# Optimization experiments

Hardware: AMD Instinct MI355X
Metric: run time of the kernel (lower is better)

## Reference

```python
import jax, jax.numpy as jnp
import numpy as np

FC = 2048      # fc_feat_size
VEMB = 512     # video_embedding_size
WEMB = 512     # word_embedding_size
H = 512        # lstm_hidden_size
A = 256        # att_hidden_size
TV = 32        # video_time_step
TC = 20        # caption_time_step
BC = 16        # batch_size_caption
RP = 32        # rp_num (proposals per caption)
B = BC * RP    # batch_size
GLOVE = 300


def setup_inputs() -> dict:
    key = jax.random.key(0)
    ks = jax.random.split(key, 12)
    def u(k, shape):
        return jax.random.uniform(k, shape, jnp.float32, -0.1, 0.1)
    def n(k, shape, s=0.05):
        return jax.random.normal(k, shape, jnp.float32) * s
    return {
        "video_fc_feat": jax.random.normal(ks[0], (B, TV, FC), jnp.float32),
        "video_caption": jax.random.normal(ks[1], (BC, TC, GLOVE), jnp.float32),
        "cap_length_list": jax.random.randint(ks[2], (BC,), 0, TC),
        # video_embedding / word_embedding (Linear layers)
        "W_vemb": u(ks[3], (VEMB, FC)), "b_vemb": jnp.zeros((VEMB,), jnp.float32),
        "W_wemb": u(ks[4], (WEMB, GLOVE)), "b_wemb": jnp.zeros((WEMB,), jnp.float32),
        # LSTMCell for video (gate order i,f,g,o as in torch)
        "Wih_v": n(ks[5], (4 * H, VEMB)), "Whh_v": n(ks[6], (4 * H, H)),
        "bih_v": jnp.zeros((4 * H,), jnp.float32), "bhh_v": jnp.zeros((4 * H,), jnp.float32),
        # LSTMCell for caption
        "Wih_c": n(ks[7], (4 * H, WEMB)), "Whh_c": n(ks[8], (4 * H, H)),
        "bih_c": jnp.zeros((4 * H,), jnp.float32), "bhh_c": jnp.zeros((4 * H,), jnp.float32),
        # attention linears
        "W_vid": u(ks[9], (A, H)), "b_vid": jnp.zeros((A,), jnp.float32),
        "W_sen": u(ks[10], (A, H)), "b_sen": jnp.zeros((A,), jnp.float32),
        "W_att": u(ks[11], (1, A)), "b_att": jnp.zeros((1,), jnp.float32),
    }


def _lstm(x_seq, Wih, Whh, bih, bhh):
    # x_seq: [B, T, D] -> hidden states [B, T, H]; torch LSTMCell gate order i,f,g,o
    Bb = x_seq.shape[0]
    Hh = Whh.shape[1]
    def step(carry, x):
        h, c = carry
        g = x @ Wih.T + bih + h @ Whh.T + bhh
        i, f, gg, o = jnp.split(g, 4, axis=-1)
        c = jax.nn.sigmoid(f) * c + jax.nn.sigmoid(i) * jnp.tanh(gg)
        h = jax.nn.sigmoid(o) * jnp.tanh(c)
        return (h, c), h
    init = (jnp.zeros((Bb, Hh), x_seq.dtype), jnp.zeros((Bb, Hh), x_seq.dtype))
    _, hs = jax.lax.scan(step, init, jnp.swapaxes(x_seq, 0, 1))
    return jnp.swapaxes(hs, 0, 1)


def reference(video_fc_feat, video_caption, cap_length_list,
              W_vemb, b_vemb, W_wemb, b_wemb,
              Wih_v, Whh_v, bih_v, bhh_v,
              Wih_c, Whh_c, bih_c, bhh_c,
              W_vid, b_vid, W_sen, b_sen, W_att, b_att):
    Bb, TVv, _ = video_fc_feat.shape
    BCc, TCc, _ = video_caption.shape
    rp = Bb // BCc
    Hh = Whh_v.shape[1]

    # caption LSTM over embedded GloVe words
    cap_x = video_caption @ W_wemb.T + b_wemb                 # [BC, TC, WEMB]
    cap_h = _lstm(cap_x, Wih_c, Whh_c, bih_c, bhh_c)          # [BC, TC, H]
    # video LSTM over embedded fc features
    vid_x = video_fc_feat @ W_vemb.T + b_vemb                 # [B, TV, VEMB]
    vid_h = _lstm(vid_x, Wih_v, Whh_v, bih_v, bhh_v)          # [B, TV, H]

    # additive attention: tanh(vid_linear(h_v) + sen_linear(h_c)) -> att_linear
    c_lin = cap_h @ W_sen.T + b_sen                           # [BC, TC, A]
    v_lin = (vid_h @ W_vid.T + b_vid).reshape(BCc, rp, TVv, -1)  # [BC, RP, TV, A]
    scores = (jnp.tanh(v_lin[:, :, :, None, :] + c_lin[:, None, None, :, :])
              @ W_att.T + b_att)[..., 0]                      # [BC, RP, TV, TC]

    # ragged masked softmax over caption length (max(len, 1) as in original)
    cap_len = jnp.maximum(cap_length_list, 1)
    mask = jnp.arange(TCc)[None, :] < cap_len[:, None]        # [BC, TC]
    m = mask[:, None, None, :]
    w = jax.nn.softmax(jnp.where(m, scores, -1e9), axis=-1)
    w = jnp.where(m, w, 0.0)                                  # [BC, RP, TV, TC]

    att_cap = jnp.einsum('brvt,bth->brvh', w, cap_h)          # [BC, RP, TV, H]
    cap_ftr_mean = att_cap.mean(axis=2)                       # mean over video steps
    vid_mean = vid_h.mean(axis=1).reshape(BCc, rp, Hh)
    return (vid_mean, cap_ftr_mean)
```

## Files before the change

### kernel.cpp

```cpp
#include <hip/hip_runtime.h>
#include <hip/hip_bf16.h>

#define FCD 2048
#define VEMBD 512
#define WEMBD 512
#define HD 512
#define AD 256
#define TVD 32
#define TCD 20
#define BCD 16
#define RPD 32
#define BD 512
#define GLOVED 300

typedef __attribute__((ext_vector_type(8))) short short8v;
typedef __attribute__((ext_vector_type(4))) float f32x4;

__device__ __forceinline__ float sigf(float x) { return 1.0f / (1.0f + __expf(-x)); }
__device__ __forceinline__ float tanhfast(float x) {
    float e = __expf(2.0f * x);
    return 1.0f - 2.0f / (e + 1.0f);
}
__device__ __forceinline__ unsigned short f2bf(float x) {
    union { __hip_bfloat16 h; unsigned short u; } v;
    v.h = __float2bfloat16(x);
    return v.u;
}
__device__ __forceinline__ float b2f(unsigned short u) {
    union { unsigned int i; float f; } v;
    v.i = ((unsigned int)u) << 16;
    return v.f;
}

__launch_bounds__(256)
__global__ void conv_f2b_kernel(const float* __restrict__ src,
                                unsigned short* __restrict__ dst, int n4) {
    for (int i = blockIdx.x * 256 + threadIdx.x; i < n4; i += gridDim.x * 256) {
        const float4 v = ((const float4*)src)[i];
        ushort4 o;
        o.x = f2bf(v.x); o.y = f2bf(v.y); o.z = f2bf(v.z); o.w = f2bf(v.w);
        ((ushort4*)dst)[i] = o;
    }
}

__launch_bounds__(256)
__global__ void conv_wcat_perm_kernel(const float* __restrict__ Wih,
                                      const float* __restrict__ Whh,
                                      unsigned short* __restrict__ Wcat) {
    const int gp = blockIdx.x;
    const int q = (gp >> 4) & 3;
    const int hc = (gp >> 6) * 16 + (gp & 15);
    const long g = (long)(q * 512 + hc);
    for (int k = threadIdx.x; k < 512; k += 256) {
        Wcat[(long)gp * 1024 + k]       = f2bf(Wih[g * 512 + k]);
        Wcat[(long)gp * 1024 + 512 + k] = f2bf(Whh[g * 512 + k]);
    }
}

__launch_bounds__(256)
__global__ void conv_bsum_kernel(const float* __restrict__ bih,
                                 const float* __restrict__ bhh,
                                 float* __restrict__ bsum) {
    const int gp = blockIdx.x * 256 + threadIdx.x;
    if (gp < 2048) {
        const int q = (gp >> 4) & 3;
        const int hc = (gp >> 6) * 16 + (gp & 15);
        const int g = q * 512 + hc;
        bsum[gp] = bih[g] + bhh[g];
    }
}

template<int AF32, int OBF>
__launch_bounds__(256)
__global__ void mfma_gemm128(const void* __restrict__ A,
                             const unsigned short* __restrict__ Bw,
                             const float* __restrict__ bias,
                             void* __restrict__ Cout,
                             int M, int N, int K)
{
    __shared__ unsigned short As[128][72];
    __shared__ unsigned short Bs[128][72];
    const int m0 = blockIdx.x * 128;
    const int n0 = blockIdx.y * 128;
    const int tid = threadIdx.x;
    const int lane = tid & 63;
    const int wid = tid >> 6;
    const int wm = (wid >> 1) * 64;
    const int wn = (wid & 1) * 64;
    const int lrow = lane & 15;
    const int lko = (lane >> 4) * 8;
    const int sr = tid >> 1;
    const int sc = (tid & 1) * 32;

    f32x4 acc[4][4] = {};

    const float* Arow_f = (const float*)A + (long)(m0 + sr) * K;
    const unsigned short* Arow_b = (const unsigned short*)A + (long)(m0 + sr) * K;
    const unsigned short* Brow = Bw + (long)(n0 + sr) * K;

    if (AF32) {
#pragma unroll
        for (int i = 0; i < 8; i++) {
            const float4 v = *(const float4*)(Arow_f + sc + i * 4);
            unsigned short* d = &As[sr][sc + i * 4];
            d[0] = f2bf(v.x); d[1] = f2bf(v.y); d[2] = f2bf(v.z); d[3] = f2bf(v.w);
        }
    } else {
#pragma unroll
        for (int i = 0; i < 4; i++)
            *(short8v*)&As[sr][sc + i * 8] = *(const short8v*)(Arow_b + sc + i * 8);
    }
#pragma unroll
    for (int i = 0; i < 4; i++)
        *(short8v*)&Bs[sr][sc + i * 8] = *(const short8v*)(Brow + sc + i * 8);
    __syncthreads();

    const int nc = K >> 6;
    float4 paf[8];
    short8v pab[4], pb[4];
    for (int c = 0; c < nc; c++) {
        if (c < nc - 1) {
            const int k0 = (c + 1) * 64;
            if (AF32) {
#pragma unroll
                for (int i = 0; i < 8; i++)
                    paf[i] = *(const float4*)(Arow_f + k0 + sc + i * 4);
            } else {
#pragma unroll
                for (int i = 0; i < 4; i++)
                    pab[i] = *(const short8v*)(Arow_b + k0 + sc + i * 8);
            }
#pragma unroll
            for (int i = 0; i < 4; i++)
                pb[i] = *(const short8v*)(Brow + k0 + sc + i * 8);
        }
#pragma unroll
        for (int kk = 0; kk < 2; kk++) {
            short8v a[4], b[4];
#pragma unroll
            for (int mi = 0; mi < 4; mi++)
                a[mi] = *(const short8v*)&As[wm + mi * 16 + lrow][kk * 32 + lko];
#pragma unroll
            for (int ni = 0; ni < 4; ni++)
                b[ni] = *(const short8v*)&Bs[wn + ni * 16 + lrow][kk * 32 + lko];
#pragma unroll
            for (int mi = 0; mi < 4; mi++)
#pragma unroll
                for (int ni = 0; ni < 4; ni++)
                    acc[mi][ni] = __builtin_amdgcn_mfma_f32_16x16x32_bf16(
                        a[mi], b[ni], acc[mi][ni], 0, 0, 0);
        }
        __syncthreads();
        if (c < nc - 1) {
            if (AF32) {
#pragma unroll
                for (int i = 0; i < 8; i++) {
                    unsigned short* d = &As[sr][sc + i * 4];
                    d[0] = f2bf(paf[i].x); d[1] = f2bf(paf[i].y);
                    d[2] = f2bf(paf[i].z); d[3] = f2bf(paf[i].w);
                }
            } else {
#pragma unroll
                for (int i = 0; i < 4; i++)
                    *(short8v*)&As[sr][sc + i * 8] = pab[i];
            }
#pragma unroll
            for (int i = 0; i < 4; i++)
                *(short8v*)&Bs[sr][sc + i * 8] = pb[i];
            __syncthreads();
        }
    }

    const int rbase = (lane >> 4) * 4;
#pragma unroll
    for (int ni = 0; ni < 4; ni++) {
        const int col = n0 + wn + ni * 16 + lrow;
        const float bv = bias[col];
#pragma unroll
        for (int mi = 0; mi < 4; mi++) {
#pragma unroll
            for (int j = 0; j < 4; j++) {
                const long row = m0 + wm + mi * 16 + rbase + j;
                const float val = acc[mi][ni][j] + bv;
                if (OBF) ((unsigned short*)Cout)[row * N + col] = f2bf(val);
                else     ((float*)Cout)[row * N + col] = val;
            }
        }
    }
}

__launch_bounds__(256, 2)
__global__ void step_fused(const unsigned short* __restrict__ vx,
                           const unsigned short* __restrict__ h_in,
                           unsigned short* __restrict__ h_out,
                           const unsigned short* __restrict__ Wcat,
                           const float* __restrict__ bsum,
                           float* __restrict__ c_state,
                           unsigned short* __restrict__ vid_h,
                           int t,
                           const float* __restrict__ xg,
                           const float* __restrict__ Whh_c,
                           const float* __restrict__ bhh_c,
                           const float* __restrict__ hc_in,
                           float* __restrict__ hc_out,
                           float* __restrict__ cap_cst,
                           float* __restrict__ cap_h)
{
    __shared__ __align__(16) unsigned char smem[26112];
    const int bx = blockIdx.x;
    const int tid = threadIdx.x;

    if (bx >= 512) {
        const int h0 = (bx - 512) * 16;
        float* Wsc = (float*)smem;
        float* Hshc = (float*)(smem + 17408);
        const int tx = tid & 15;
        const int ty = tid >> 4;
        const int lrow2 = tid >> 2;
        const int lq = tid & 3;
        float acc4[4] = {};

        for (int k0 = 0; k0 < 512; k0 += 64) {
            {
                const int q = lrow2 >> 4;
                const int hcc = lrow2 & 15;
                const float* src = Whh_c + (long)(q * 512 + h0 + hcc) * 512 + k0 + lq * 16;
                const int col = hcc * 4 + q;
#pragma unroll
                for (int j = 0; j < 4; j++) {
                    const float4 v = *(const float4*)(src + j * 4);
                    Wsc[(lq * 16 + j * 4 + 0) * 68 + col] = v.x;
                    Wsc[(lq * 16 + j * 4 + 1) * 68 + col] = v.y;
                    Wsc[(lq * 16 + j * 4 + 2) * 68 + col] = v.z;
                    Wsc[(lq * 16 + j * 4 + 3) * 68 + col] = v.w;
                }
            }
            {
                const int lb = tid >> 4;
                const int lk4 = (tid & 15) * 4;
                *(float4*)&Hshc[lb * 68 + lk4] = *(const float4*)(hc_in + (long)lb * 512 + k0 + lk4);
            }
            __syncthreads();
#pragma unroll
            for (int kq = 0; kq < 16; kq++) {
                const float4 h4 = *(const float4*)&Hshc[ty * 68 + kq * 4];
                const float4 w0 = *(const float4*)&Wsc[(kq * 4 + 0) * 68 + tx * 4];
                const float4 w1 = *(const float4*)&Wsc[(kq * 4 + 1) * 68 + tx * 4];
                const float4 w2 = *(const float4*)&Wsc[(kq * 4 + 2) * 68 + tx * 4];
                const float4 w3 = *(const float4*)&Wsc[(kq * 4 + 3) * 68 + tx * 4];
                acc4[0] += h4.x * w0.x + h4.y * w1.x + h4.z * w2.x + h4.w * w3.x;
                acc4[1] += h4.x * w0.y + h4.y * w1.y + h4.z * w2.y + h4.w * w3.y;
                acc4[2] += h4.x * w0.z + h4.y * w1.z + h4.z * w2.z + h4.w * w3.z;
                acc4[3] += h4.x * w0.w + h4.y * w1.w + h4.z * w2.w + h4.w * w3.w;
            }
            __syncthreads();
        }
        const int hc = h0 + tx;
        const long xrow = (long)(ty * TCD + t) * 2048;
        const float gi = acc4[0] + xg[xrow + hc]        + bhh_c[hc];
        const float gf = acc4[1] + xg[xrow + 512 + hc]  + bhh_c[512 + hc];
        const float gg = acc4[2] + xg[xrow + 1024 + hc] + bhh_c[1024 + hc];
        const float go = acc4[3] + xg[xrow + 1536 + hc] + bhh_c[1536 + hc];
        const float c_old = cap_cst[(long)ty * 512 + hc];
        const float ii = sigf(gi), ff = sigf(gf), g2 = tanhfast(gg), oo = sigf(go);
        const float c = ff * c_old + ii * g2;
        const float h = oo * tanhfast(c);
        cap_cst[(long)ty * 512 + hc] = c;
        hc_out[(long)ty * 512 + hc] = h;
        cap_h[(long)(ty * TCD + t) * 512 + hc] = h;
        return;
    }

    const int n0 = (bx & 31) * 64;
    const int b0 = (bx >> 5) * 32;
    const int lane = tid & 63;
    const int w = tid >> 6;
    const int bi = w & 1;
    const int nq = w >> 1;
    const int lrow = lane & 15;
    const int lko = (lane >> 4) * 8;
    const int sra = tid >> 3;
    const int sca = (tid & 7) * 16;

    unsigned short* As = (unsigned short*)smem;
    unsigned short* Ws = (unsigned short*)(smem + 8704);

    const unsigned short* arow_vx = vx + ((long)(b0 + sra) * TVD + t) * 512;
    const unsigned short* arow_h  = h_in + (long)(b0 + sra) * 512;
    const unsigned short* wrow0   = Wcat + (long)(n0 + sra) * 1024;
    const unsigned short* wrow1   = Wcat + (long)(n0 + sra + 32) * 1024;

    f32x4 acc[2] = {};

    *(short8v*)&As[sra * 136 + sca]     = *(const short8v*)(arow_vx + sca);
    *(short8v*)&As[sra * 136 + sca + 8] = *(const short8v*)(arow_vx + sca + 8);
    *(short8v*)&Ws[sra * 136 + sca]            = *(const short8v*)(wrow0 + sca);
    *(short8v*)&Ws[sra * 136 + sca + 8]        = *(const short8v*)(wrow0 + sca + 8);
    *(short8v*)&Ws[(sra + 32) * 136 + sca]     = *(const short8v*)(wrow1 + sca);
    *(short8v*)&Ws[(sra + 32) * 136 + sca + 8] = *(const short8v*)(wrow1 + sca + 8);
    __syncthreads();

    short8v pa0, pa1, pw0, pw1, pw2, pw3;
    for (int c = 0; c < 8; c++) {
        if (c < 7) {
            const int k0 = (c + 1) * 128;
            const unsigned short* ap = (k0 < 512) ? (arow_vx + k0) : (arow_h + (k0 - 512));
            pa0 = *(const short8v*)(ap + sca);
            pa1 = *(const short8v*)(ap + sca + 8);
            pw0 = *(const short8v*)(wrow0 + k0 + sca);
            pw1 = *(const short8v*)(wrow0 + k0 + sca + 8);
            pw2 = *(const short8v*)(wrow1 + k0 + sca);
            pw3 = *(const short8v*)(wrow1 + k0 + sca + 8);
        }
#pragma unroll
        for (int kk = 0; kk < 4; kk++) {
            const short8v a = *(const short8v*)&As[(bi * 16 + lrow) * 136 + kk * 32 + lko];
#pragma unroll
            for (int nl = 0; nl < 2; nl++) {
                const short8v b = *(const short8v*)&Ws[((nq * 2 + nl) * 16 + lrow) * 136 + kk * 32 + lko];
                acc[nl] = __builtin_amdgcn_mfma_f32_16x16x32_bf16(a, b, acc[nl], 0, 0, 0);
            }
        }
        __syncthreads();
        if (c < 7) {
            *(short8v*)&As[sra * 136 + sca]            = pa0;
            *(short8v*)&As[sra * 136 + sca + 8]        = pa1;
            *(short8v*)&Ws[sra * 136 + sca]            = pw0;
            *(short8v*)&Ws[sra * 136 + sca + 8]        = pw1;
            *(short8v*)&Ws[(sra + 32) * 136 + sca]     = pw2;
            *(short8v*)&Ws[(sra + 32) * 136 + sca + 8] = pw3;
            __syncthreads();
        }
    }

    float* red = (float*)smem;
    const int rbase = (lane >> 4) * 4;
    if (w >= 2) {
#pragma unroll
        for (int nl = 0; nl < 2; nl++)
#pragma unroll
            for (int j = 0; j < 4; j++)
                red[nl * 512 + (bi * 16 + rbase + j) * 16 + lrow] = acc[nl][j];
    }
    __syncthreads();
    if (w < 2) {
        const int hc = (n0 >> 2) + lrow;
        const float bs0 = bsum[n0 + lrow];
        const float bs1 = bsum[n0 + 16 + lrow];
        const float bs2 = bsum[n0 + 32 + lrow];
        const float bs3 = bsum[n0 + 48 + lrow];
#pragma unroll
        for (int j = 0; j < 4; j++) {
            const int blocal = bi * 16 + rbase + j;
            const long b = b0 + blocal;
            const float gi = acc[0][j] + bs0;
            const float gf = acc[1][j] + bs1;
            const float gg = red[blocal * 16 + lrow] + bs2;
            const float go = red[512 + blocal * 16 + lrow] + bs3;
            const float c_old = c_state[b * 512 + hc];
            const float ii = sigf(gi), ff = sigf(gf), g2 = tanhfast(gg), oo = sigf(go);
            const float cn = ff * c_old + ii * g2;
            const float h = oo * tanhfast(cn);
            c_state[b * 512 + hc] = cn;
            h_out[b * 512 + hc] = f2bf(h);
            vid_h[(b * TVD + t) * 512 + hc] = f2bf(h);
        }
    }
}

__launch_bounds__(256)
__global__ void gemm_bias_kernel(const float* __restrict__ A,
                                 const float* __restrict__ Bw,
                                 const float* __restrict__ bias,
                                 float* __restrict__ C,
                                 int M, int N, int K) {
    __shared__ float As[16][68];
    __shared__ float Bs[16][68];
    const int n0 = blockIdx.x * 64;
    const int m0 = blockIdx.y * 64;
    const int tid = threadIdx.x;
    const int tx = tid & 15;
    const int ty = tid >> 4;
    const int lrow = tid >> 2;
    const int lk4 = (tid & 3) * 4;

    float acc[4][4] = {};

    for (int k0 = 0; k0 < K; k0 += 16) {
        {
            const float* src = A + (long)(m0 + lrow) * K + k0 + lk4;
            float4 v;
            if (k0 + 16 <= K) v = *(const float4*)src;
            else {
                v.x = (k0 + lk4 + 0 < K) ? src[0] : 0.f;
                v.y = (k0 + lk4 + 1 < K) ? src[1] : 0.f;
                v.z = (k0 + lk4 + 2 < K) ? src[2] : 0.f;
                v.w = (k0 + lk4 + 3 < K) ? src[3] : 0.f;
            }
            As[lk4 + 0][lrow] = v.x; As[lk4 + 1][lrow] = v.y;
            As[lk4 + 2][lrow] = v.z; As[lk4 + 3][lrow] = v.w;
        }
        {
            const float* src = Bw + (long)(n0 + lrow) * K + k0 + lk4;
            float4 v;
            if (k0 + 16 <= K) v = *(const float4*)src;
            else {
                v.x = (k0 + lk4 + 0 < K) ? src[0] : 0.f;
                v.y = (k0 + lk4 + 1 < K) ? src[1] : 0.f;
                v.z = (k0 + lk4 + 2 < K) ? src[2] : 0.f;
                v.w = (k0 + lk4 + 3 < K) ? src[3] : 0.f;
            }
            Bs[lk4 + 0][lrow] = v.x; Bs[lk4 + 1][lrow] = v.y;
            Bs[lk4 + 2][lrow] = v.z; Bs[lk4 + 3][lrow] = v.w;
        }
        __syncthreads();
#pragma unroll
        for (int kk = 0; kk < 16; kk++) {
            const float4 av = *(const float4*)&As[kk][ty * 4];
            const float4 bv = *(const float4*)&Bs[kk][tx * 4];
            acc[0][0] += av.x * bv.x; acc[0][1] += av.x * bv.y; acc[0][2] += av.x * bv.z; acc[0][3] += av.x * bv.w;
            acc[1][0] += av.y * bv.x; acc[1][1] += av.y * bv.y; acc[1][2] += av.y * bv.z; acc[1][3] += av.y * bv.w;
            acc[2][0] += av.z * bv.x; acc[2][1] += av.z * bv.y; acc[2][2] += av.z * bv.z; acc[2][3] += av.z * bv.w;
            acc[3][0] += av.w * bv.x; acc[3][1] += av.w * bv.y; acc[3][2] += av.w * bv.z; acc[3][3] += av.w * bv.w;
        }
        __syncthreads();
    }

    const float b0v = bias[n0 + tx * 4 + 0];
    const float b1v = bias[n0 + tx * 4 + 1];
    const float b2v = bias[n0 + tx * 4 + 2];
    const float b3v = bias[n0 + tx * 4 + 3];
#pragma unroll
    for (int i = 0; i < 4; i++) {
        float* dst = C + (long)(m0 + ty * 4 + i) * N + n0 + tx * 4;
        dst[0] = acc[i][0] + b0v;
        dst[1] = acc[i][1] + b1v;
        dst[2] = acc[i][2] + b2v;
        dst[3] = acc[i][3] + b3v;
    }
}

#define PFL 258
__launch_bounds__(256, 2)
__global__ void attn_kernel(const float* __restrict__ v_lin,
                            const float* __restrict__ c_lin,
                            const float* __restrict__ W_att,
                            const float* __restrict__ b_att,
                            const int* __restrict__ cap_len,
                            const float* __restrict__ cap_h,
                            float* __restrict__ out2)
{
    const int br = blockIdx.x;
    const int bc = br >> 5;
    const int tid = threadIdx.x;
    __shared__ float cl[TCD][PFL];
    __shared__ float vl[TVD][PFL];
    __shared__ float wa[AD];
    __shared__ float sl[TVD][TCD];
    __shared__ float wsum[TCD];

    {
        const float* csrc = c_lin + (long)bc * TCD * AD;
        for (int idx = tid; idx < TCD * 128; idx += 256) {
            const int row = idx >> 7, c2 = (idx & 127) * 2;
            *(float2*)&cl[row][c2] = *(const float2*)(csrc + row * AD + c2);
        }
        const float* vsrc = v_lin + (long)br * TVD * AD;
        for (int idx = tid; idx < TVD * 128; idx += 256) {
            const int row = idx >> 7, c2 = (idx & 127) * 2;
            *(float2*)&vl[row][c2] = *(const float2*)(vsrc + row * AD + c2);
        }
        wa[tid] = W_att[tid];
    }
    const float batt = b_att[0];
    __syncthreads();

    {
        const int v = tid & 31;
        const int tg = tid >> 5;
        const int t0 = tg, t1 = tg + 8, t2 = tg + 16;
        const bool ok2 = (t2 < TCD);
        const int t2c = ok2 ? t2 : 0;
        float s0 = 0.f, s1 = 0.f, s2 = 0.f;
#pragma unroll 4
        for (int i = 0; i < 128; i++) {
            const float2 w2 = *(const float2*)&wa[2 * i];
            const float2 vv = *(const float2*)&vl[v][2 * i];
            const float2 c0 = *(const float2*)&cl[t0][2 * i];
            const float2 c1 = *(const float2*)&cl[t1][2 * i];
            const float2 c2 = *(const float2*)&cl[t2c][2 * i];
            s0 += tanhfast(vv.x + c0.x) * w2.x + tanhfast(vv.y + c0.y) * w2.y;
            s1 += tanhfast(vv.x + c1.x) * w2.x + tanhfast(vv.y + c1.y) * w2.y;
            s2 += tanhfast(vv.x + c2.x) * w2.x + tanhfast(vv.y + c2.y) * w2.y;
        }
        sl[v][t0] = s0 + batt;
        sl[v][t1] = s1 + batt;
        if (ok2) sl[v][t2] = s2 + batt;
    }
    __syncthreads();

    int L = cap_len[bc];
    if (L < 1) L = 1;
    if (tid < TVD) {
        const int v = tid;
        float m = -1e30f;
        for (int t = 0; t < TCD; t++)
            if (t < L) m = fmaxf(m, sl[v][t]);
        float sum = 0.f;
        for (int t = 0; t < TCD; t++)
            if (t < L) sum += __expf(sl[v][t] - m);
        const float inv = 1.f / sum;
        for (int t = 0; t < TCD; t++)
            sl[v][t] = (t < L) ? __expf(sl[v][t] - m) * inv : 0.f;
    }
    __syncthreads();
    if (tid < TCD) {
        float s = 0.f;
        for (int v = 0; v < TVD; v++) s += sl[v][tid];
        wsum[tid] = s * (1.0f / TVD);
    }
    __syncthreads();

    const float* chb = cap_h + (long)bc * TCD * HD;
#pragma unroll
    for (int r = 0; r < 2; r++) {
        const int h = r * 256 + tid;
        float s = 0.f;
#pragma unroll
        for (int t = 0; t < TCD; t++)
            s += wsum[t] * chb[t * HD + h];
        out2[(long)br * HD + h] = s;
    }
}

__launch_bounds__(256)
__global__ void vidmean_bf_kernel(const unsigned short* __restrict__ vid_h,
                                  float* __restrict__ out1)
{
    const int idx = blockIdx.x * 256 + threadIdx.x;
    const int b = idx >> 6;
    const int h8 = (idx & 63) * 8;
    float s[8] = {};
    for (int t = 0; t < TVD; t++) {
        const short8v v = *(const short8v*)(vid_h + ((long)b * TVD + t) * 512 + h8);
#pragma unroll
        for (int j = 0; j < 8; j++) s[j] += b2f((unsigned short)v[j]);
    }
#pragma unroll
    for (int j = 0; j < 8; j++)
        out1[(long)b * 512 + h8 + j] = s[j] * (1.0f / TVD);
}

extern "C" void kernel_launch(void* const* d_in, const int* in_sizes, int n_in,
                              void* d_out, int out_size, void* d_ws, size_t ws_size,
                              hipStream_t stream) {
    const float* video_fc      = (const float*)d_in[0];
    const float* video_caption = (const float*)d_in[1];
    const int*   cap_len       = (const int*)d_in[2];
    const float* W_vemb = (const float*)d_in[3];
    const float* b_vemb = (const float*)d_in[4];
    const float* W_wemb = (const float*)d_in[5];
    const float* b_wemb = (const float*)d_in[6];
    const float* Wih_v  = (const float*)d_in[7];
    const float* Whh_v  = (const float*)d_in[8];
    const float* bih_v  = (const float*)d_in[9];
    const float* bhh_v  = (const float*)d_in[10];
    const float* Wih_c  = (const float*)d_in[11];
    const float* Whh_c  = (const float*)d_in[12];
    const float* bih_c  = (const float*)d_in[13];
    const float* bhh_c  = (const float*)d_in[14];
    const float* W_vid  = (const float*)d_in[15];
    const float* b_vid  = (const float*)d_in[16];
    const float* W_sen  = (const float*)d_in[17];
    const float* b_sen  = (const float*)d_in[18];
    const float* W_att  = (const float*)d_in[19];
    const float* b_att  = (const float*)d_in[20];

    float* out1 = (float*)d_out;
    float* out2 = out1 + BD * HD;

    float* ws = (float*)d_ws;
    size_t off = 0;
    auto alloc = [&](size_t nfloats) {
        float* p = ws + off;
        off += (nfloats + 63) & ~(size_t)63;
        return p;
    };
    unsigned short* vidx_bf = (unsigned short*)alloc((size_t)BD * TVD * VEMBD / 2);
    unsigned short* vidh_bf = (unsigned short*)alloc((size_t)BD * TVD * HD / 2);
    unsigned short* h_bf_a  = (unsigned short*)alloc((size_t)BD * HD / 2);
    unsigned short* h_bf_b  = (unsigned short*)alloc((size_t)BD * HD / 2);
    float* c_st    = alloc((size_t)BD * HD);
    float* v_lin   = alloc((size_t)BD * TVD * AD);
    unsigned short* Wvemb_bf = (unsigned short*)alloc((size_t)VEMBD * FCD / 2);
    unsigned short* Wvid_bf  = (unsigned short*)alloc((size_t)AD * HD / 2);
    unsigned short* Wcat_bf  = (unsigned short*)alloc((size_t)2048 * 1024 / 2);
    float* bsum    = alloc(2048);
    float* cap_x   = alloc((size_t)BCD * TCD * WEMBD);
    float* xg_c    = alloc((size_t)BCD * TCD * 4 * HD);
    float* cap_h   = alloc((size_t)BCD * TCD * HD);
    float* c_lin   = alloc((size_t)BCD * TCD * AD);
    float* cap_ha  = alloc((size_t)BCD * HD);
    float* cap_hb  = alloc((size_t)BCD * HD);
    float* cap_cst = alloc((size_t)BCD * HD);
    const size_t fcn = (size_t)BD * TVD * FCD;
    const bool preconv = ((off + fcn / 2 + 64) * sizeof(float) <= ws_size);
    unsigned short* vidfc_bf = preconv ? (unsigned short*)alloc(fcn / 2) : nullptr;

    hipMemsetAsync(h_bf_a, 0, (size_t)BD * HD * sizeof(unsigned short), stream);
    hipMemsetAsync(c_st, 0, (size_t)BD * HD * sizeof(float), stream);
    hipMemsetAsync(cap_ha, 0, (size_t)BCD * HD * sizeof(float), stream);
    hipMemsetAsync(cap_cst, 0, (size_t)BCD * HD * sizeof(float), stream);

    conv_f2b_kernel<<<512, 256, 0, stream>>>(W_vemb, Wvemb_bf, VEMBD * FCD / 4);
    conv_f2b_kernel<<<128, 256, 0, stream>>>(W_vid, Wvid_bf, AD * HD / 4);
    conv_wcat_perm_kernel<<<2048, 256, 0, stream>>>(Wih_v, Whh_v, Wcat_bf);
    conv_bsum_kernel<<<8, 256, 0, stream>>>(bih_v, bhh_v, bsum);

    gemm_bias_kernel<<<dim3(WEMBD / 64, (BCD * TCD) / 64), 256, 0, stream>>>(
        video_caption, W_wemb, b_wemb, cap_x, BCD * TCD, WEMBD, GLOVED);
    gemm_bias_kernel<<<dim3((4 * HD) / 64, (BCD * TCD) / 64), 256, 0, stream>>>(
        cap_x, Wih_c, bih_c, xg_c, BCD * TCD, 4 * HD, WEMBD);

    if (preconv) {
        conv_f2b_kernel<<<2048, 256, 0, stream>>>(video_fc, vidfc_bf, (int)(fcn / 4));
        mfma_gemm128<0, 1><<<dim3((BD * TVD) / 128, VEMBD / 128), 256, 0, stream>>>(
            vidfc_bf, Wvemb_bf, b_vemb, vidx_bf, BD * TVD, VEMBD, FCD);
    } else {
        mfma_gemm128<1, 1><<<dim3((BD * TVD) / 128, VEMBD / 128), 256, 0, stream>>>(
            video_fc, Wvemb_bf, b_vemb, vidx_bf, BD * TVD, VEMBD, FCD);
    }

    for (int t = 0; t < TVD; t++) {
        const unsigned short* hin = (t & 1) ? h_bf_b : h_bf_a;
        unsigned short* hout = (t & 1) ? h_bf_a : h_bf_b;
        const float* chin = (t & 1) ? cap_hb : cap_ha;
        float* chout = (t & 1) ? cap_ha : cap_hb;
        const int nblk = (t < TCD) ? 544 : 512;
        step_fused<<<nblk, 256, 0, stream>>>(
            vidx_bf, hin, hout, Wcat_bf, bsum, c_st, vidh_bf, t,
            xg_c, Whh_c, bhh_c, chin, chout, cap_cst, cap_h);
    }

    gemm_bias_kernel<<<dim3(AD / 64, (BCD * TCD) / 64), 256, 0, stream>>>(
        cap_h, W_sen, b_sen, c_lin, BCD * TCD, AD, HD);
    mfma_gemm128<0, 0><<<dim3((BD * TVD) / 128, AD / 128), 256, 0, stream>>>(
        vidh_bf, Wvid_bf, b_vid, v_lin, BD * TVD, AD, HD);

    attn_kernel<<<BD, 256, 0, stream>>>(v_lin, c_lin, W_att, b_att, cap_len, cap_h, out2);
    vidmean_bf_kernel<<<(BD * HD / 8) / 256, 256, 0, stream>>>(vidh_bf, out1);
}
```

Baseline: 818.7 us.

## Hoist video LSTM input projection out of recurrent loop into one batched GEMM

Computes the input-to-hidden gate contribution (x @ Wih^T + biases) for all 32 video time steps at once with a single large MFMA GEMM before the recurrence. Each per-step fused kernel then only multiplies h by Whh (K=512 instead of 1024) and adds the precomputed fp32 gates. This halves the serial per-step matmul work. In exchange it writes and reads a large fp32 gate buffer (B*TV*2048 floats, about 128 MB), which adds memory traffic and workspace.

```diff
diff --git a/kernel.cpp b/kernel.cpp
--- a/kernel.cpp
+++ b/kernel.cpp
@@ -76,7 +76,7 @@
                              const unsigned short* __restrict__ Bw,
                              const float* __restrict__ bias,
                              void* __restrict__ Cout,
-                             int M, int N, int K)
+                             int M, int N, int K, int ldb)
 {
     __shared__ unsigned short As[128][72];
     __shared__ unsigned short Bs[128][72];
@@ -96,7 +96,7 @@
 
     const float* Arow_f = (const float*)A + (long)(m0 + sr) * K;
     const unsigned short* Arow_b = (const unsigned short*)A + (long)(m0 + sr) * K;
-    const unsigned short* Brow = Bw + (long)(n0 + sr) * K;
+    const unsigned short* Brow = Bw + (long)(n0 + sr) * ldb;
 
     if (AF32) {
 #pragma unroll
@@ -190,11 +190,10 @@
 }
 
 __launch_bounds__(256, 2)
-__global__ void step_fused(const unsigned short* __restrict__ vx,
+__global__ void step_fused(const float* __restrict__ xg_v,
                            const unsigned short* __restrict__ h_in,
                            unsigned short* __restrict__ h_out,
                            const unsigned short* __restrict__ Wcat,
-                           const float* __restrict__ bsum,
                            float* __restrict__ c_state,
                            unsigned short* __restrict__ vid_h,
                            int t,
@@ -285,15 +284,14 @@
     unsigned short* As = (unsigned short*)smem;
     unsigned short* Ws = (unsigned short*)(smem + 8704);
 
-    const unsigned short* arow_vx = vx + ((long)(b0 + sra) * TVD + t) * 512;
-    const unsigned short* arow_h  = h_in + (long)(b0 + sra) * 512;
-    const unsigned short* wrow0   = Wcat + (long)(n0 + sra) * 1024;
-    const unsigned short* wrow1   = Wcat + (long)(n0 + sra + 32) * 1024;
+    const unsigned short* arow_h = h_in + (long)(b0 + sra) * 512;
+    const unsigned short* wrow0  = Wcat + (long)(n0 + sra) * 1024 + 512;
+    const unsigned short* wrow1  = Wcat + (long)(n0 + sra + 32) * 1024 + 512;
 
     f32x4 acc[2] = {};
 
-    *(short8v*)&As[sra * 136 + sca]     = *(const short8v*)(arow_vx + sca);
-    *(short8v*)&As[sra * 136 + sca + 8] = *(const short8v*)(arow_vx + sca + 8);
+    *(short8v*)&As[sra * 136 + sca]     = *(const short8v*)(arow_h + sca);
+    *(short8v*)&As[sra * 136 + sca + 8] = *(const short8v*)(arow_h + sca + 8);
     *(short8v*)&Ws[sra * 136 + sca]            = *(const short8v*)(wrow0 + sca);
     *(short8v*)&Ws[sra * 136 + sca + 8]        = *(const short8v*)(wrow0 + sca + 8);
     *(short8v*)&Ws[(sra + 32) * 136 + sca]     = *(const short8v*)(wrow1 + sca);
@@ -301,12 +299,11 @@
     __syncthreads();
 
     short8v pa0, pa1, pw0, pw1, pw2, pw3;
-    for (int c = 0; c < 8; c++) {
-        if (c < 7) {
+    for (int c = 0; c < 4; c++) {
+        if (c < 3) {
             const int k0 = (c + 1) * 128;
-            const unsigned short* ap = (k0 < 512) ? (arow_vx + k0) : (arow_h + (k0 - 512));
-            pa0 = *(const short8v*)(ap + sca);
-            pa1 = *(const short8v*)(ap + sca + 8);
+            pa0 = *(const short8v*)(arow_h + k0 + sca);
+            pa1 = *(const short8v*)(arow_h + k0 + sca + 8);
             pw0 = *(const short8v*)(wrow0 + k0 + sca);
             pw1 = *(const short8v*)(wrow0 + k0 + sca + 8);
             pw2 = *(const short8v*)(wrow1 + k0 + sca);
@@ -322,7 +319,7 @@
             }
         }
         __syncthreads();
-        if (c < 7) {
+        if (c < 3) {
             *(short8v*)&As[sra * 136 + sca]            = pa0;
             *(short8v*)&As[sra * 136 + sca + 8]        = pa1;
             *(short8v*)&Ws[sra * 136 + sca]            = pw0;
@@ -345,18 +342,15 @@
     __syncthreads();
     if (w < 2) {
         const int hc = (n0 >> 2) + lrow;
-        const float bs0 = bsum[n0 + lrow];
-        const float bs1 = bsum[n0 + 16 + lrow];
-        const float bs2 = bsum[n0 + 32 + lrow];
-        const float bs3 = bsum[n0 + 48 + lrow];
 #pragma unroll
         for (int j = 0; j < 4; j++) {
             const int blocal = bi * 16 + rbase + j;
             const long b = b0 + blocal;
-            const float gi = acc[0][j] + bs0;
-            const float gf = acc[1][j] + bs1;
-            const float gg = red[blocal * 16 + lrow] + bs2;
-            const float go = red[512 + blocal * 16 + lrow] + bs3;
+            const float* xr = xg_v + ((long)b * TVD + t) * 2048 + n0 + lrow;
+            const float gi = acc[0][j] + xr[0];
+            const float gf = acc[1][j] + xr[16];
+            const float gg = red[blocal * 16 + lrow] + xr[32];
+            const float go = red[512 + blocal * 16 + lrow] + xr[48];
             const float c_old = c_state[b * 512 + hc];
             const float ii = sigf(gi), ff = sigf(gf), g2 = tanhfast(gg), oo = sigf(go);
             const float cn = ff * c_old + ii * g2;
@@ -603,6 +597,7 @@
     float* cap_ha  = alloc((size_t)BCD * HD);
     float* cap_hb  = alloc((size_t)BCD * HD);
     float* cap_cst = alloc((size_t)BCD * HD);
+    float* xg_v    = alloc((size_t)BD * TVD * 4 * HD);
     const size_t fcn = (size_t)BD * TVD * FCD;
     const bool preconv = ((off + fcn / 2 + 64) * sizeof(float) <= ws_size);
     unsigned short* vidfc_bf = preconv ? (unsigned short*)alloc(fcn / 2) : nullptr;
@@ -625,11 +620,14 @@
     if (preconv) {
         conv_f2b_kernel<<<2048, 256, 0, stream>>>(video_fc, vidfc_bf, (int)(fcn / 4));
         mfma_gemm128<0, 1><<<dim3((BD * TVD) / 128, VEMBD / 128), 256, 0, stream>>>(
-            vidfc_bf, Wvemb_bf, b_vemb, vidx_bf, BD * TVD, VEMBD, FCD);
+            vidfc_bf, Wvemb_bf, b_vemb, vidx_bf, BD * TVD, VEMBD, FCD, FCD);
     } else {
         mfma_gemm128<1, 1><<<dim3((BD * TVD) / 128, VEMBD / 128), 256, 0, stream>>>(
-            video_fc, Wvemb_bf, b_vemb, vidx_bf, BD * TVD, VEMBD, FCD);
-    }
+            video_fc, Wvemb_bf, b_vemb, vidx_bf, BD * TVD, VEMBD, FCD, FCD);
+    }
+
+    mfma_gemm128<0, 0><<<dim3((BD * TVD) / 128, 2048 / 128), 256, 0, stream>>>(
+        vidx_bf, Wcat_bf, bsum, xg_v, BD * TVD, 2048, HD, 1024);
 
     for (int t = 0; t < TVD; t++) {
         const unsigned short* hin = (t & 1) ? h_bf_b : h_bf_a;
@@ -638,14 +636,14 @@
         float* chout = (t & 1) ? cap_ha : cap_hb;
         const int nblk = (t < TCD) ? 544 : 512;
         step_fused<<<nblk, 256, 0, stream>>>(
-            vidx_bf, hin, hout, Wcat_bf, bsum, c_st, vidh_bf, t,
+            xg_v, hin, hout, Wcat_bf, c_st, vidh_bf, t,
             xg_c, Whh_c, bhh_c, chin, chout, cap_cst, cap_h);
     }
 
     gemm_bias_kernel<<<dim3(AD / 64, (BCD * TCD) / 64), 256, 0, stream>>>(
         cap_h, W_sen, b_sen, c_lin, BCD * TCD, AD, HD);
     mfma_gemm128<0, 0><<<dim3((BD * TVD) / 128, AD / 128), 256, 0, stream>>>(
-        vidh_bf, Wvid_bf, b_vid, v_lin, BD * TVD, AD, HD);
+        vidh_bf, Wvid_bf, b_vid, v_lin, BD * TVD, AD, HD, HD);
 
     attn_kernel<<<BD, 256, 0, stream>>>(v_lin, c_lin, W_att, b_att, cap_len, cap_h, out2);
     vidmean_bf_kernel<<<(BD * HD / 8) / 256, 256, 0, stream>>>(vidh_bf, out1);
```

Result: slower. 886.4 us (+8.3%).

## Halve batch tile per block in fused LSTM step to double grid size

Applied to the files above, without the earlier changes.

The fused video LSTM step kernel now handles 16 batch rows per block instead of 32, so the grid doubles to 1024 video blocks plus the caption blocks. Each warp computes one 16x16 gate tile, and the f/g/o gates are reduced through shared memory to warp 0. This is meant to raise occupancy and parallelism on the many-CU GPU for this latency-bound recurrent step. The cost is that each weight tile is reloaded by twice as many blocks, and more of the work sits in the serial epilogue on warp 0.

```diff
diff --git a/kernel.cpp b/kernel.cpp
--- a/kernel.cpp
+++ b/kernel.cpp
@@ -206,12 +206,12 @@
                            float* __restrict__ cap_cst,
                            float* __restrict__ cap_h)
 {
-    __shared__ __align__(16) unsigned char smem[26112];
+    __shared__ __align__(16) unsigned char smem[21760];
     const int bx = blockIdx.x;
     const int tid = threadIdx.x;
 
-    if (bx >= 512) {
-        const int h0 = (bx - 512) * 16;
+    if (bx >= 1024) {
+        const int h0 = (bx - 1024) * 16;
         float* Wsc = (float*)smem;
         float* Hshc = (float*)(smem + 17408);
         const int tx = tid & 15;
@@ -272,78 +272,66 @@
     }
 
     const int n0 = (bx & 31) * 64;
-    const int b0 = (bx >> 5) * 32;
+    const int b0 = (bx >> 5) * 16;
     const int lane = tid & 63;
     const int w = tid >> 6;
-    const int bi = w & 1;
-    const int nq = w >> 1;
     const int lrow = lane & 15;
     const int lko = (lane >> 4) * 8;
-    const int sra = tid >> 3;
-    const int sca = (tid & 7) * 16;
+    const int sra = tid >> 4;
+    const int sca = (tid & 15) * 8;
+    const int srw = tid >> 2;
+    const int scw = (tid & 3) * 32;
 
     unsigned short* As = (unsigned short*)smem;
-    unsigned short* Ws = (unsigned short*)(smem + 8704);
+    unsigned short* Ws = (unsigned short*)(smem + 4352);
+    float* red = (float*)smem;
 
     const unsigned short* arow_vx = vx + ((long)(b0 + sra) * TVD + t) * 512;
     const unsigned short* arow_h  = h_in + (long)(b0 + sra) * 512;
-    const unsigned short* wrow0   = Wcat + (long)(n0 + sra) * 1024;
-    const unsigned short* wrow1   = Wcat + (long)(n0 + sra + 32) * 1024;
-
-    f32x4 acc[2] = {};
-
-    *(short8v*)&As[sra * 136 + sca]     = *(const short8v*)(arow_vx + sca);
-    *(short8v*)&As[sra * 136 + sca + 8] = *(const short8v*)(arow_vx + sca + 8);
-    *(short8v*)&Ws[sra * 136 + sca]            = *(const short8v*)(wrow0 + sca);
-    *(short8v*)&Ws[sra * 136 + sca + 8]        = *(const short8v*)(wrow0 + sca + 8);
-    *(short8v*)&Ws[(sra + 32) * 136 + sca]     = *(const short8v*)(wrow1 + sca);
-    *(short8v*)&Ws[(sra + 32) * 136 + sca + 8] = *(const short8v*)(wrow1 + sca + 8);
+    const unsigned short* wrow    = Wcat + (long)(n0 + srw) * 1024;
+
+    f32x4 acc = {};
+
+    *(short8v*)&As[sra * 136 + sca] = *(const short8v*)(arow_vx + sca);
+#pragma unroll
+    for (int i = 0; i < 4; i++)
+        *(short8v*)&Ws[srw * 136 + scw + i * 8] = *(const short8v*)(wrow + scw + i * 8);
     __syncthreads();
 
-    short8v pa0, pa1, pw0, pw1, pw2, pw3;
+    short8v pa, pw[4];
     for (int c = 0; c < 8; c++) {
         if (c < 7) {
             const int k0 = (c + 1) * 128;
             const unsigned short* ap = (k0 < 512) ? (arow_vx + k0) : (arow_h + (k0 - 512));
-            pa0 = *(const short8v*)(ap + sca);
-            pa1 = *(const short8v*)(ap + sca + 8);
-            pw0 = *(const short8v*)(wrow0 + k0 + sca);
-            pw1 = *(const short8v*)(wrow0 + k0 + sca + 8);
-            pw2 = *(const short8v*)(wrow1 + k0 + sca);
-            pw3 = *(const short8v*)(wrow1 + k0 + sca + 8);
+            pa = *(const short8v*)(ap + sca);
+#pragma unroll
+            for (int i = 0; i < 4; i++)
+                pw[i] = *(const short8v*)(wrow + k0 + scw + i * 8);
         }
 #pragma unroll
         for (int kk = 0; kk < 4; kk++) {
-            const short8v a = *(const short8v*)&As[(bi * 16 + lrow) * 136 + kk * 32 + lko];
-#pragma unroll
-            for (int nl = 0; nl < 2; nl++) {
-                const short8v b = *(const short8v*)&Ws[((nq * 2 + nl) * 16 + lrow) * 136 + kk * 32 + lko];
-                acc[nl] = __builtin_amdgcn_mfma_f32_16x16x32_bf16(a, b, acc[nl], 0, 0, 0);
-            }
+            const short8v a = *(const short8v*)&As[lrow * 136 + kk * 32 + lko];
+            const short8v b = *(const short8v*)&Ws[(w * 16 + lrow) * 136 + kk * 32 + lko];
+            acc = __builtin_amdgcn_mfma_f32_16x16x32_bf16(a, b, acc, 0, 0, 0);
         }
         __syncthreads();
         if (c < 7) {
-            *(short8v*)&As[sra * 136 + sca]            = pa0;
-            *(short8v*)&As[sra * 136 + sca + 8]        = pa1;
-            *(short8v*)&Ws[sra * 136 + sca]            = pw0;
-            *(short8v*)&Ws[sra * 136 + sca + 8]        = pw1;
-            *(short8v*)&Ws[(sra + 32) * 136 + sca]     = pw2;
-            *(short8v*)&Ws[(sra + 32) * 136 + sca + 8] = pw3;
+            *(short8v*)&As[sra * 136 + sca] = pa;
+#pragma unroll
+            for (int i = 0; i < 4; i++)
+                *(short8v*)&Ws[srw * 136 + scw + i * 8] = pw[i];
             __syncthreads();
         }
     }
 
-    float* red = (float*)smem;
     const int rbase = (lane >> 4) * 4;
-    if (w >= 2) {
-#pragma unroll
-        for (int nl = 0; nl < 2; nl++)
-#pragma unroll
-            for (int j = 0; j < 4; j++)
-                red[nl * 512 + (bi * 16 + rbase + j) * 16 + lrow] = acc[nl][j];
+    if (w >= 1) {
+#pragma unroll
+        for (int j = 0; j < 4; j++)
+            red[(w - 1) * 256 + (rbase + j) * 16 + lrow] = acc[j];
     }
     __syncthreads();
-    if (w < 2) {
+    if (w == 0) {
         const int hc = (n0 >> 2) + lrow;
         const float bs0 = bsum[n0 + lrow];
         const float bs1 = bsum[n0 + 16 + lrow];
@@ -351,12 +339,12 @@
         const float bs3 = bsum[n0 + 48 + lrow];
 #pragma unroll
         for (int j = 0; j < 4; j++) {
-            const int blocal = bi * 16 + rbase + j;
+            const int blocal = rbase + j;
             const long b = b0 + blocal;
-            const float gi = acc[0][j] + bs0;
-            const float gf = acc[1][j] + bs1;
-            const float gg = red[blocal * 16 + lrow] + bs2;
-            const float go = red[512 + blocal * 16 + lrow] + bs3;
+            const float gi = acc[j] + bs0;
+            const float gf = red[0 * 256 + blocal * 16 + lrow] + bs1;
+            const float gg = red[1 * 256 + blocal * 16 + lrow] + bs2;
+            const float go = red[2 * 256 + blocal * 16 + lrow] + bs3;
             const float c_old = c_state[b * 512 + hc];
             const float ii = sigf(gi), ff = sigf(gf), g2 = tanhfast(gg), oo = sigf(go);
             const float cn = ff * c_old + ii * g2;
@@ -636,7 +624,7 @@
         unsigned short* hout = (t & 1) ? h_bf_a : h_bf_b;
         const float* chin = (t & 1) ? cap_hb : cap_ha;
         float* chout = (t & 1) ? cap_ha : cap_hb;
-        const int nblk = (t < TCD) ? 544 : 512;
+        const int nblk = (t < TCD) ? 1056 : 1024;
         step_fused<<<nblk, 256, 0, stream>>>(
             vidx_bf, hin, hout, Wcat_bf, bsum, c_st, vidh_bf, t,
             xg_c, Whh_c, bhh_c, chin, chout, cap_cst, cap_h);
```

Result: slower. 974.9 us (+19.1%).
